# Kernel tuning notes

Hardware: AMD Instinct MI355X
Metric: run time of the kernel (lower is better)

Reference implementation:

```python
import jax, jax.numpy as jnp
import numpy as np

B, N, C, H = 4, 2048, 1024, 16
D = C // H

def setup_inputs() -> dict:
    key = jax.random.key(0)
    k1, k2, k3 = jax.random.split(key, 3)
    x = jax.random.normal(k1, (B, N, C), dtype=jnp.float32)
    w_qkv = jax.random.normal(k2, (C, 3 * C), dtype=jnp.float32) * (C ** -0.5)
    w_proj = jax.random.normal(k3, (C, C), dtype=jnp.float32) * (C ** -0.5)
    b_proj = jnp.zeros((C,), dtype=jnp.float32)
    return {"x": x, "w_qkv": w_qkv, "w_proj": w_proj, "b_proj": b_proj}

def reference(x, w_qkv, w_proj, b_proj):
    scale = D ** -0.5
    qkv = x @ w_qkv                                   # [B,N,3C]
    qkv = qkv.reshape(B, N, 3, H, D).transpose(2, 0, 3, 1, 4)  # [3,B,H,N,D]
    q, k, v = qkv[0], qkv[1], qkv[2]
    attn = jnp.einsum('bhnd,bhmd->bhnm', q, k) * scale  # [B,H,N,N]
    attn = jax.nn.softmax(attn, axis=-1)
    o = jnp.einsum('bhnm,bhmd->bhnd', attn, v)          # [B,H,N,D]
    o = o.transpose(0, 2, 1, 3).reshape(B, N, C)
    return o @ w_proj + b_proj
```

## Files before the change

kernel.cpp:

```cpp
#include <hip/hip_runtime.h>
#include <hip/hip_bf16.h>


#define B_ 4
#define N_ 2048
#define C_ 1024
#define H_ 16
#define D_ 64
#define MCONST 24.0f

typedef __attribute__((ext_vector_type(8))) __bf16 bf16x8;
typedef __attribute__((ext_vector_type(4))) float f32x4;
typedef __attribute__((ext_vector_type(16))) float f32x16;
typedef unsigned int u32;
typedef __attribute__((ext_vector_type(2))) u32 u32x2;
typedef __attribute__((ext_vector_type(4))) u32 u32x4;

__device__ inline unsigned short f2bf(float f) {
  __bf16 h = (__bf16)f;
  return __builtin_bit_cast(unsigned short, h);
}

__device__ __forceinline__ u32 pk2(float lo, float hi) {
  return (u32)f2bf(lo) | ((u32)f2bf(hi) << 16);
}

__device__ __forceinline__ void gld16(const void* g, void* l) {
  __builtin_amdgcn_global_load_lds(
      (const __attribute__((address_space(1))) u32*)g,
      (__attribute__((address_space(3))) u32*)l, 16, 0, 0);
}

__global__ __launch_bounds__(256) void cvt_bf16_kernel(
    const float* __restrict__ in, unsigned short* __restrict__ out) {
  int i = (blockIdx.x * 256 + threadIdx.x) * 8;
  float4 f0 = *(const float4*)&in[i];
  float4 f1 = *(const float4*)&in[i + 4];
  ushort4 h0, h1;
  h0.x = f2bf(f0.x); h0.y = f2bf(f0.y); h0.z = f2bf(f0.z); h0.w = f2bf(f0.w);
  h1.x = f2bf(f1.x); h1.y = f2bf(f1.y); h1.z = f2bf(f1.z); h1.w = f2bf(f1.w);
  *(ushort4*)&out[i] = h0;
  *(ushort4*)&out[i + 4] = h1;
}

__global__ __launch_bounds__(256) void transpose_cvt_kernel(
    const float* __restrict__ in, unsigned short* __restrict__ out,
    int K, int Nn) {
  __shared__ float tile[32][33];
  const int t = threadIdx.x;
  const int k0 = blockIdx.y * 32, n0 = blockIdx.x * 32;
  {
    int r = t >> 3, c = (t & 7) * 4;
    float4 f = *(const float4*)&in[(size_t)(k0 + r) * Nn + n0 + c];
    tile[r][c + 0] = f.x; tile[r][c + 1] = f.y;
    tile[r][c + 2] = f.z; tile[r][c + 3] = f.w;
  }
  __syncthreads();
  {
    int nr = t >> 3, kc = (t & 7) * 4;
    ushort4 h;
    h.x = f2bf(tile[kc + 0][nr]);
    h.y = f2bf(tile[kc + 1][nr]);
    h.z = f2bf(tile[kc + 2][nr]);
    h.w = f2bf(tile[kc + 3][nr]);
    *(ushort4*)&out[(size_t)(n0 + nr) * K + k0 + kc] = h;
  }
}

__global__ __launch_bounds__(256) void transpose_v_kernel(
    const unsigned short* __restrict__ vb, unsigned short* __restrict__ vtb) {
  __shared__ u32 tile[64][65];
  const int tid = threadIdx.x;
  const int n0 = blockIdx.x * 64;
  const int bh = blockIdx.y;
  const size_t base = (size_t)bh * N_ * D_;
#pragma unroll
  for (int i = 0; i < 2; i++) {
    int id = i * 256 + tid;
    int row = id >> 3, c8 = id & 7;
    uint4 v = *(const uint4*)&vb[base + (size_t)(n0 + row) * D_ + c8 * 8];
    const unsigned short* pv = (const unsigned short*)&v;
#pragma unroll
    for (int j = 0; j < 8; j++) tile[row][c8 * 8 + j] = pv[j];
  }
  __syncthreads();
#pragma unroll
  for (int i = 0; i < 2; i++) {
    int id = i * 256 + tid;
    int d = id >> 3, nc = id & 7;
    uint4 o;
    unsigned short* po = (unsigned short*)&o;
#pragma unroll
    for (int j = 0; j < 8; j++) po[j] = (unsigned short)tile[nc * 8 + j][d];
    *(uint4*)&vtb[base + (size_t)d * N_ + n0 + nc * 8] = o;
  }
}

__global__ __launch_bounds__(512, 1) void gemm256_kernel(
    const unsigned short* __restrict__ A, const unsigned short* __restrict__ Bt,
    unsigned short* __restrict__ qb, unsigned short* __restrict__ kb,
    unsigned short* __restrict__ vb, int M, int K, int Nout)
{
  __shared__ unsigned short LDS[3][2][256 * 32];
  const int tid = threadIdx.x;
  const int w = tid >> 6, lane = tid & 63;
  const int l15 = lane & 15, lk = lane >> 4;
  const int wm = w >> 2, wn = w & 3;
  const int n0 = blockIdx.x * 256, m0 = blockIdx.y * 256;

  const int s_row = tid >> 2;
  const int s_col = ((tid & 3) * 8) ^ (((s_row >> 3) & 1) * 16);
  const int s_dst = tid * 8;
  const int kcol = (lk * 8) ^ (((l15 >> 3) & 1) * 16);

  f32x4 acc[8][4];
#pragma unroll
  for (int m = 0; m < 8; m++)
#pragma unroll
    for (int n = 0; n < 4; n++) acc[m][n] = f32x4{0.f, 0.f, 0.f, 0.f};

#pragma unroll
  for (int i = 0; i < 2; i++)
    gld16(&A[(size_t)(m0 + i * 128 + s_row) * K + s_col],
          &LDS[0][0][i * 4096 + s_dst]);
#pragma unroll
  for (int i = 0; i < 2; i++)
    gld16(&Bt[(size_t)(n0 + i * 128 + s_row) * K + s_col],
          &LDS[0][1][i * 4096 + s_dst]);

  int cur = 0;
  for (int j = 0; j < 31; ++j) {
    const int nxt = (cur + 1 == 3) ? 0 : cur + 1;
    const int kt = (j + 1) * 32;
#pragma unroll
    for (int i = 0; i < 2; i++)
      gld16(&A[(size_t)(m0 + i * 128 + s_row) * K + kt + s_col],
            &LDS[nxt][0][i * 4096 + s_dst]);
    asm volatile("s_waitcnt vmcnt(2)" ::: "memory");
    __builtin_amdgcn_s_barrier();
    asm volatile("" ::: "memory");

    bf16x8 bf[4], af[4];
#pragma unroll
    for (int n = 0; n < 4; n++)
      bf[n] = *(const bf16x8*)&LDS[cur][1][(wn * 64 + n * 16 + l15) * 32 + kcol];
#pragma unroll
    for (int m = 0; m < 4; m++)
      af[m] = *(const bf16x8*)&LDS[cur][0][(wm * 128 + m * 16 + l15) * 32 + kcol];
    __builtin_amdgcn_s_setprio(1);
#pragma unroll
    for (int m = 0; m < 4; m++)
#pragma unroll
      for (int n = 0; n < 4; n++)
        acc[m][n] = __builtin_amdgcn_mfma_f32_16x16x32_bf16(af[m], bf[n], acc[m][n], 0, 0, 0);
    __builtin_amdgcn_s_setprio(0);

#pragma unroll
    for (int i = 0; i < 2; i++)
      gld16(&Bt[(size_t)(n0 + i * 128 + s_row) * K + kt + s_col],
            &LDS[nxt][1][i * 4096 + s_dst]);

#pragma unroll
    for (int m = 0; m < 4; m++)
      af[m] = *(const bf16x8*)&LDS[cur][0][(wm * 128 + (m + 4) * 16 + l15) * 32 + kcol];
    __builtin_amdgcn_s_setprio(1);
#pragma unroll
    for (int m = 0; m < 4; m++)
#pragma unroll
      for (int n = 0; n < 4; n++)
        acc[m + 4][n] = __builtin_amdgcn_mfma_f32_16x16x32_bf16(af[m], bf[n], acc[m + 4][n], 0, 0, 0);
    __builtin_amdgcn_s_setprio(0);
    cur = nxt;
  }

  asm volatile("s_waitcnt vmcnt(0)" ::: "memory");
  __builtin_amdgcn_s_barrier();
  asm volatile("" ::: "memory");
  {
    bf16x8 bf[4], af[4];
#pragma unroll
    for (int n = 0; n < 4; n++)
      bf[n] = *(const bf16x8*)&LDS[cur][1][(wn * 64 + n * 16 + l15) * 32 + kcol];
#pragma unroll
    for (int m = 0; m < 4; m++)
      af[m] = *(const bf16x8*)&LDS[cur][0][(wm * 128 + m * 16 + l15) * 32 + kcol];
#pragma unroll
    for (int m = 0; m < 4; m++)
#pragma unroll
      for (int n = 0; n < 4; n++)
        acc[m][n] = __builtin_amdgcn_mfma_f32_16x16x32_bf16(af[m], bf[n], acc[m][n], 0, 0, 0);
#pragma unroll
    for (int m = 0; m < 4; m++)
      af[m] = *(const bf16x8*)&LDS[cur][0][(wm * 128 + (m + 4) * 16 + l15) * 32 + kcol];
#pragma unroll
    for (int m = 0; m < 4; m++)
#pragma unroll
      for (int n = 0; n < 4; n++)
        acc[m + 4][n] = __builtin_amdgcn_mfma_f32_16x16x32_bf16(af[m], bf[n], acc[m + 4][n], 0, 0, 0);
  }

#pragma unroll
  for (int n = 0; n < 4; n++) {
    int c = n0 + wn * 64 + n * 16 + l15;
    int tsel = c >> 10, h = (c >> 6) & 15, d = c & 63;
    unsigned short* dst = (tsel == 0) ? qb : (tsel == 1 ? kb : vb);
    float sc = (tsel == 0) ? 0.125f * 1.44269504088896340736f : 1.0f;
#pragma unroll
    for (int m = 0; m < 8; m++) {
#pragma unroll
      for (int r = 0; r < 4; r++) {
        int row = m0 + wm * 128 + m * 16 + lk * 4 + r;
        int b = row >> 11, nn = row & 2047;
        dst[(((size_t)(b * 16 + h)) * 2048 + nn) * 64 + d] = f2bf(acc[m][n][r] * sc);
      }
    }
  }
}

__global__ __launch_bounds__(256) void gemm128_kernel(
    const unsigned short* __restrict__ A, const unsigned short* __restrict__ Bt,
    const float* __restrict__ bias, float* __restrict__ outp,
    int M, int K, int Nout)
{
  __shared__ unsigned short Al[128 * 64];
  __shared__ unsigned short Bl[128 * 64];
  const int tid = threadIdx.x;
  const int w = tid >> 6, lane = tid & 63;
  const int l15 = lane & 15, lk = lane >> 4;
  const int wr = w >> 1, wc = w & 1;
  const int n0 = blockIdx.x * 128, m0 = blockIdx.y * 128;
  const int srow = tid >> 3;
  const int scol = (tid & 7) * 8;

  f32x4 acc[4][4];
#pragma unroll
  for (int m = 0; m < 4; m++)
#pragma unroll
    for (int n = 0; n < 4; n++) acc[m][n] = f32x4{0.f, 0.f, 0.f, 0.f};

  for (int kt = 0; kt < K; kt += 64) {
#pragma unroll
    for (int i = 0; i < 4; i++)
      gld16(&A[(size_t)(m0 + i * 32 + srow) * K + kt + scol],
            &Al[i * 2048 + w * 512]);
#pragma unroll
    for (int i = 0; i < 4; i++)
      gld16(&Bt[(size_t)(n0 + i * 32 + srow) * K + kt + scol],
            &Bl[i * 2048 + w * 512]);
    __syncthreads();

#pragma unroll
    for (int kk = 0; kk < 2; kk++) {
      bf16x8 af[4], bf[4];
#pragma unroll
      for (int m = 0; m < 4; m++)
        af[m] = *(const bf16x8*)&Al[(wr * 64 + m * 16 + l15) * 64 + kk * 32 + lk * 8];
#pragma unroll
      for (int n = 0; n < 4; n++)
        bf[n] = *(const bf16x8*)&Bl[(wc * 64 + n * 16 + l15) * 64 + kk * 32 + lk * 8];
#pragma unroll
      for (int m = 0; m < 4; m++)
#pragma unroll
        for (int n = 0; n < 4; n++)
          acc[m][n] = __builtin_amdgcn_mfma_f32_16x16x32_bf16(af[m], bf[n], acc[m][n], 0, 0, 0);
    }
    __syncthreads();
  }

#pragma unroll
  for (int n = 0; n < 4; n++) {
    int c = n0 + wc * 64 + n * 16 + l15;
    float bv = bias[c];
#pragma unroll
    for (int m = 0; m < 4; m++) {
#pragma unroll
      for (int r = 0; r < 4; r++) {
        int row = m0 + wr * 64 + m * 16 + lk * 4 + r;
        outp[(size_t)row * Nout + c] = acc[m][n][r] + bv;
      }
    }
  }
}

__global__ __launch_bounds__(512) void flash_kernel(
    const unsigned short* __restrict__ qb, const unsigned short* __restrict__ kb,
    const unsigned short* __restrict__ vtb, unsigned short* __restrict__ ob)
{
  __shared__ unsigned short KVs[2][2][2][64 * 64];
  __shared__ float Lf[2][128];
  float* scratch = (float*)&KVs[0][0][0][0];

  const int tid = threadIdx.x;
  const int w = tid >> 6;
  const int lane = tid & 63;
  const int l31 = lane & 31;
  const int hi = lane >> 5;
  const int g = w >> 2;
  const int ws = w & 3;
  const int q0 = blockIdx.x * 128;
  const int bh = blockIdx.y;
  const size_t base = (size_t)bh * N_ * D_;
  const unsigned short* Qg = qb + base;
  const unsigned short* Kg = kb + base;
  const unsigned short* Vtg = vtb + base;

  const int t8 = tid & 255;
  const int s_r = t8 >> 3;
  const int s_sl = (t8 & 7) ^ (s_r & 7);
  const int swz = (lane & 7) << 3;

  const int qrow_g = q0 + ws * 32 + l31;
  bf16x8 qf[4];
#pragma unroll
  for (int ds = 0; ds < 4; ds++)
    qf[ds] = *(const bf16x8*)&Qg[(size_t)qrow_g * 64 + ds * 16 + hi * 8];

  f32x16 acc0, acc1, minit;
#pragma unroll
  for (int i = 0; i < 16; i++) { acc0[i] = 0.f; acc1[i] = 0.f; minit[i] = -MCONST; }
  float lrow = 0.f;

  const int kvbeg = g * (N_ / 2);

#pragma unroll
  for (int i = 0; i < 2; i++)
    gld16(&Kg[(size_t)(kvbeg + i * 32 + s_r) * 64 + s_sl * 8],
          &KVs[g][0][0][i * 2048 + ws * 512]);
#pragma unroll
  for (int i = 0; i < 2; i++)
    gld16(&Vtg[(size_t)(i * 32 + s_r) * N_ + kvbeg + s_sl * 8],
          &KVs[g][0][1][i * 2048 + ws * 512]);

  int cur = 0;
  for (int it = 0; it < 16; ++it) {
    __syncthreads();

    if (it + 1 < 16) {
      int kvn = kvbeg + (it + 1) * 64;
#pragma unroll
      for (int i = 0; i < 2; i++)
        gld16(&Kg[(size_t)(kvn + i * 32 + s_r) * 64 + s_sl * 8],
              &KVs[g][cur ^ 1][0][i * 2048 + ws * 512]);
#pragma unroll
      for (int i = 0; i < 2; i++)
        gld16(&Vtg[(size_t)(i * 32 + s_r) * N_ + kvn + s_sl * 8],
              &KVs[g][cur ^ 1][1][i * 2048 + ws * 512]);
    }

    const unsigned short* Kl = &KVs[g][cur][0][0];
    const unsigned short* Vl = &KVs[g][cur][1][0];

    u32 F[4][4];
#pragma unroll
    for (int t = 0; t < 2; t++) {
      f32x16 sa = minit;
      __builtin_amdgcn_s_setprio(1);
#pragma unroll
      for (int ds = 0; ds < 4; ds++) {
        bf16x8 a = *(const bf16x8*)&Kl[(t * 32 + l31) * 64 + ((ds * 16 + hi * 8) ^ swz)];
        sa = __builtin_amdgcn_mfma_f32_32x32x16_bf16(a, qf[ds], sa, 0, 0, 0);
      }
      __builtin_amdgcn_s_setprio(0);

      float p[16];
#pragma unroll
      for (int r = 0; r < 16; r++) p[r] = __builtin_amdgcn_exp2f(sa[r]);
      lrow += ((p[0] + p[1]) + (p[2] + p[3])) + ((p[4] + p[5]) + (p[6] + p[7]))
            + ((p[8] + p[9]) + (p[10] + p[11])) + ((p[12] + p[13]) + (p[14] + p[15]));

      u32 pk[8];
#pragma unroll
      for (int j = 0; j < 8; j++) pk[j] = pk2(p[2 * j], p[2 * j + 1]);
#if __has_builtin(__builtin_amdgcn_permlane32_swap)
      u32x2 r02 = __builtin_amdgcn_permlane32_swap(pk[0], pk[2], false, false);
      u32x2 r13 = __builtin_amdgcn_permlane32_swap(pk[1], pk[3], false, false);
      u32x2 r46 = __builtin_amdgcn_permlane32_swap(pk[4], pk[6], false, false);
      u32x2 r57 = __builtin_amdgcn_permlane32_swap(pk[5], pk[7], false, false);
      F[2 * t][0] = r02[0]; F[2 * t][2] = r02[1];
      F[2 * t][1] = r13[0]; F[2 * t][3] = r13[1];
      F[2 * t + 1][0] = r46[0]; F[2 * t + 1][2] = r46[1];
      F[2 * t + 1][1] = r57[0]; F[2 * t + 1][3] = r57[1];
#else
      u32 sw[8];
#pragma unroll
      for (int j = 0; j < 8; j++) sw[j] = (u32)__shfl_xor((int)pk[j], 32);
      F[2 * t][0] = hi ? sw[2] : pk[0];
      F[2 * t][1] = hi ? sw[3] : pk[1];
      F[2 * t][2] = hi ? pk[2] : sw[0];
      F[2 * t][3] = hi ? pk[3] : sw[1];
      F[2 * t + 1][0] = hi ? sw[6] : pk[4];
      F[2 * t + 1][1] = hi ? sw[7] : pk[5];
      F[2 * t + 1][2] = hi ? pk[6] : sw[4];
      F[2 * t + 1][3] = hi ? pk[7] : sw[5];
#endif
    }

    __builtin_amdgcn_s_setprio(1);
#pragma unroll
    for (int ks = 0; ks < 4; ks++) {
      u32x4 fv = {F[ks][0], F[ks][1], F[ks][2], F[ks][3]};
      bf16x8 a = __builtin_bit_cast(bf16x8, fv);
      bf16x8 b0 = *(const bf16x8*)&Vl[(0 * 32 + l31) * 64 + ((ks * 16 + hi * 8) ^ swz)];
      acc0 = __builtin_amdgcn_mfma_f32_32x32x16_bf16(a, b0, acc0, 0, 0, 0);
      bf16x8 b1 = *(const bf16x8*)&Vl[(1 * 32 + l31) * 64 + ((ks * 16 + hi * 8) ^ swz)];
      acc1 = __builtin_amdgcn_mfma_f32_32x32x16_bf16(a, b1, acc1, 0, 0, 0);
    }
    __builtin_amdgcn_s_setprio(0);
    cur ^= 1;
  }

  float rs = lrow + __shfl_xor(lrow, 32);
  if (lane < 32) Lf[g][ws * 32 + l31] = rs;
  __syncthreads();

  if (g == 0) {
#pragma unroll
    for (int r = 0; r < 16; r++) {
      int qr = (r & 3) + 8 * (r >> 2) + 4 * hi;
      scratch[(ws * 32 + qr) * 64 + l31]      = acc0[r];
      scratch[(ws * 32 + qr) * 64 + 32 + l31] = acc1[r];
    }
  }
  __syncthreads();
  if (g == 1) {
    const int b = bh >> 4, h = bh & 15;
#pragma unroll
    for (int r = 0; r < 16; r++) {
      int qr = (r & 3) + 8 * (r >> 2) + 4 * hi;
      float inv = 1.0f / (Lf[0][ws * 32 + qr] + Lf[1][ws * 32 + qr]);
      float o0 = scratch[(ws * 32 + qr) * 64 + l31]      + acc0[r];
      float o1 = scratch[(ws * 32 + qr) * 64 + 32 + l31] + acc1[r];
      int nq = q0 + ws * 32 + qr;
      size_t ob0 = (((size_t)b * N_ + nq) * H_ + h) * D_;
      ob[ob0 + l31]      = f2bf(o0 * inv);
      ob[ob0 + 32 + l31] = f2bf(o1 * inv);
    }
  }
}

extern "C" void kernel_launch(void* const* d_in, const int* in_sizes, int n_in,
                              void* d_out, int out_size, void* d_ws, size_t ws_size,
                              hipStream_t stream) {
  const float* x      = (const float*)d_in[0];
  const float* w_qkv  = (const float*)d_in[1];
  const float* w_proj = (const float*)d_in[2];
  const float* b_proj = (const float*)d_in[3];
  float* out = (float*)d_out;

  const size_t qsz = (size_t)B_ * H_ * N_ * D_;
  unsigned short* qb     = (unsigned short*)d_ws;
  unsigned short* kb     = qb + qsz;
  unsigned short* vb     = kb + qsz;
  unsigned short* vtb    = vb + qsz;
  unsigned short* xbf    = vtb + qsz;
  unsigned short* ob     = xbf;
  unsigned short* wqkv_t = xbf + qsz;
  unsigned short* wproj_t= wqkv_t + (size_t)3072 * 1024;

  cvt_bf16_kernel<<<4096, 256, 0, stream>>>(x, xbf);
  transpose_cvt_kernel<<<dim3(3072 / 32, 1024 / 32), 256, 0, stream>>>(w_qkv, wqkv_t, 1024, 3072);
  transpose_cvt_kernel<<<dim3(1024 / 32, 1024 / 32), 256, 0, stream>>>(w_proj, wproj_t, 1024, 1024);

  gemm256_kernel<<<dim3(3072 / 256, 8192 / 256), 512, 0, stream>>>(
      xbf, wqkv_t, qb, kb, vb, 8192, 1024, 3072);

  transpose_v_kernel<<<dim3(N_ / 64, B_ * H_), 256, 0, stream>>>(vb, vtb);

  flash_kernel<<<dim3(N_ / 128, B_ * H_), 512, 0, stream>>>(qb, kb, vtb, ob);

  gemm128_kernel<<<dim3(1024 / 128, 8192 / 128), 256, 0, stream>>>(
      ob, wproj_t, b_proj, out, 8192, 1024, 1024);
}
```

Before: 217.4 us.

## Fuse V transpose into QKV GEMM epilogue and pipeline projection GEMM

New measurement: 212.6 us. -2.2%, faster.

```diff
diff --git a/kernel.cpp b/kernel.cpp
--- a/kernel.cpp
+++ b/kernel.cpp
@@ -8,6 +8,7 @@
 #define H_ 16
 #define D_ 64
 #define MCONST 24.0f
+#define QSCALE (0.125f * 1.44269504088896340736f)
 
 typedef __attribute__((ext_vector_type(8))) __bf16 bf16x8;
 typedef __attribute__((ext_vector_type(4))) float f32x4;
@@ -67,39 +68,10 @@
   }
 }
 
-__global__ __launch_bounds__(256) void transpose_v_kernel(
-    const unsigned short* __restrict__ vb, unsigned short* __restrict__ vtb) {
-  __shared__ u32 tile[64][65];
-  const int tid = threadIdx.x;
-  const int n0 = blockIdx.x * 64;
-  const int bh = blockIdx.y;
-  const size_t base = (size_t)bh * N_ * D_;
-#pragma unroll
-  for (int i = 0; i < 2; i++) {
-    int id = i * 256 + tid;
-    int row = id >> 3, c8 = id & 7;
-    uint4 v = *(const uint4*)&vb[base + (size_t)(n0 + row) * D_ + c8 * 8];
-    const unsigned short* pv = (const unsigned short*)&v;
-#pragma unroll
-    for (int j = 0; j < 8; j++) tile[row][c8 * 8 + j] = pv[j];
-  }
-  __syncthreads();
-#pragma unroll
-  for (int i = 0; i < 2; i++) {
-    int id = i * 256 + tid;
-    int d = id >> 3, nc = id & 7;
-    uint4 o;
-    unsigned short* po = (unsigned short*)&o;
-#pragma unroll
-    for (int j = 0; j < 8; j++) po[j] = (unsigned short)tile[nc * 8 + j][d];
-    *(uint4*)&vtb[base + (size_t)d * N_ + n0 + nc * 8] = o;
-  }
-}
-
 __global__ __launch_bounds__(512, 1) void gemm256_kernel(
     const unsigned short* __restrict__ A, const unsigned short* __restrict__ Bt,
     unsigned short* __restrict__ qb, unsigned short* __restrict__ kb,
-    unsigned short* __restrict__ vb, int M, int K, int Nout)
+    unsigned short* __restrict__ vtb, int M, int K, int Nout)
 {
   __shared__ unsigned short LDS[3][2][256 * 32];
   const int tid = threadIdx.x;
@@ -203,34 +175,48 @@
   for (int n = 0; n < 4; n++) {
     int c = n0 + wn * 64 + n * 16 + l15;
     int tsel = c >> 10, h = (c >> 6) & 15, d = c & 63;
-    unsigned short* dst = (tsel == 0) ? qb : (tsel == 1 ? kb : vb);
-    float sc = (tsel == 0) ? 0.125f * 1.44269504088896340736f : 1.0f;
-#pragma unroll
-    for (int m = 0; m < 8; m++) {
-#pragma unroll
-      for (int r = 0; r < 4; r++) {
-        int row = m0 + wm * 128 + m * 16 + lk * 4 + r;
-        int b = row >> 11, nn = row & 2047;
-        dst[(((size_t)(b * 16 + h)) * 2048 + nn) * 64 + d] = f2bf(acc[m][n][r] * sc);
+    if (tsel < 2) {
+      unsigned short* dst = (tsel == 0) ? qb : kb;
+      float sc = (tsel == 0) ? QSCALE : 1.0f;
+#pragma unroll
+      for (int m = 0; m < 8; m++) {
+#pragma unroll
+        for (int r = 0; r < 4; r++) {
+          int row = m0 + wm * 128 + m * 16 + lk * 4 + r;
+          int b = row >> 11, nn = row & 2047;
+          dst[(((size_t)(b * 16 + h)) * 2048 + nn) * 64 + d] = f2bf(acc[m][n][r] * sc);
+        }
       }
-    }
-  }
-}
-
-__global__ __launch_bounds__(256) void gemm128_kernel(
+    } else {
+#pragma unroll
+      for (int m = 0; m < 8; m++) {
+        int row0 = m0 + wm * 128 + m * 16 + lk * 4;
+        int b = row0 >> 11, nn = row0 & 2047;
+        ushort4 pv;
+        pv.x = f2bf(acc[m][n][0]); pv.y = f2bf(acc[m][n][1]);
+        pv.z = f2bf(acc[m][n][2]); pv.w = f2bf(acc[m][n][3]);
+        *(ushort4*)&vtb[(((size_t)(b * 16 + h)) * 64 + d) * 2048 + nn] = pv;
+      }
+    }
+  }
+}
+
+__global__ __launch_bounds__(512, 1) void gemmproj_kernel(
     const unsigned short* __restrict__ A, const unsigned short* __restrict__ Bt,
     const float* __restrict__ bias, float* __restrict__ outp,
     int M, int K, int Nout)
 {
-  __shared__ unsigned short Al[128 * 64];
-  __shared__ unsigned short Bl[128 * 64];
+  __shared__ unsigned short LDS[3][12288];
   const int tid = threadIdx.x;
   const int w = tid >> 6, lane = tid & 63;
   const int l15 = lane & 15, lk = lane >> 4;
-  const int wr = w >> 1, wc = w & 1;
-  const int n0 = blockIdx.x * 128, m0 = blockIdx.y * 128;
-  const int srow = tid >> 3;
-  const int scol = (tid & 7) * 8;
+  const int wm = w >> 1, wn = w & 1;
+  const int n0 = blockIdx.x * 128, m0 = blockIdx.y * 256;
+
+  const int s_row = tid >> 2;
+  const int s_col = ((tid & 3) * 8) ^ (((s_row >> 3) & 1) * 16);
+  const int s_dst = tid * 8;
+  const int kcol = (lk * 8) ^ (((l15 >> 3) & 1) * 16);
 
   f32x4 acc[4][4];
 #pragma unroll
@@ -238,44 +224,89 @@
 #pragma unroll
     for (int n = 0; n < 4; n++) acc[m][n] = f32x4{0.f, 0.f, 0.f, 0.f};
 
-  for (int kt = 0; kt < K; kt += 64) {
-#pragma unroll
-    for (int i = 0; i < 4; i++)
-      gld16(&A[(size_t)(m0 + i * 32 + srow) * K + kt + scol],
-            &Al[i * 2048 + w * 512]);
-#pragma unroll
-    for (int i = 0; i < 4; i++)
-      gld16(&Bt[(size_t)(n0 + i * 32 + srow) * K + kt + scol],
-            &Bl[i * 2048 + w * 512]);
-    __syncthreads();
-
-#pragma unroll
-    for (int kk = 0; kk < 2; kk++) {
-      bf16x8 af[4], bf[4];
-#pragma unroll
-      for (int m = 0; m < 4; m++)
-        af[m] = *(const bf16x8*)&Al[(wr * 64 + m * 16 + l15) * 64 + kk * 32 + lk * 8];
-#pragma unroll
-      for (int n = 0; n < 4; n++)
-        bf[n] = *(const bf16x8*)&Bl[(wc * 64 + n * 16 + l15) * 64 + kk * 32 + lk * 8];
-#pragma unroll
-      for (int m = 0; m < 4; m++)
-#pragma unroll
-        for (int n = 0; n < 4; n++)
-          acc[m][n] = __builtin_amdgcn_mfma_f32_16x16x32_bf16(af[m], bf[n], acc[m][n], 0, 0, 0);
-    }
-    __syncthreads();
+#pragma unroll
+  for (int i = 0; i < 2; i++)
+    gld16(&A[(size_t)(m0 + i * 128 + s_row) * K + s_col],
+          &LDS[0][i * 4096 + s_dst]);
+  gld16(&Bt[(size_t)(n0 + s_row) * K + s_col], &LDS[0][8192 + s_dst]);
+
+  int cur = 0;
+  for (int j = 0; j < 31; ++j) {
+    const int nxt = (cur + 1 == 3) ? 0 : cur + 1;
+    const int kt = (j + 1) * 32;
+#pragma unroll
+    for (int i = 0; i < 2; i++)
+      gld16(&A[(size_t)(m0 + i * 128 + s_row) * K + kt + s_col],
+            &LDS[nxt][i * 4096 + s_dst]);
+    asm volatile("s_waitcnt vmcnt(2)" ::: "memory");
+    __builtin_amdgcn_s_barrier();
+    asm volatile("" ::: "memory");
+
+    bf16x8 bf[4], af[2];
+#pragma unroll
+    for (int n = 0; n < 4; n++)
+      bf[n] = *(const bf16x8*)&LDS[cur][8192 + (wn * 64 + n * 16 + l15) * 32 + kcol];
+#pragma unroll
+    for (int m = 0; m < 2; m++)
+      af[m] = *(const bf16x8*)&LDS[cur][(wm * 64 + m * 16 + l15) * 32 + kcol];
+    __builtin_amdgcn_s_setprio(1);
+#pragma unroll
+    for (int m = 0; m < 2; m++)
+#pragma unroll
+      for (int n = 0; n < 4; n++)
+        acc[m][n] = __builtin_amdgcn_mfma_f32_16x16x32_bf16(af[m], bf[n], acc[m][n], 0, 0, 0);
+    __builtin_amdgcn_s_setprio(0);
+
+    gld16(&Bt[(size_t)(n0 + s_row) * K + kt + s_col], &LDS[nxt][8192 + s_dst]);
+
+#pragma unroll
+    for (int m = 0; m < 2; m++)
+      af[m] = *(const bf16x8*)&LDS[cur][(wm * 64 + (m + 2) * 16 + l15) * 32 + kcol];
+    __builtin_amdgcn_s_setprio(1);
+#pragma unroll
+    for (int m = 0; m < 2; m++)
+#pragma unroll
+      for (int n = 0; n < 4; n++)
+        acc[m + 2][n] = __builtin_amdgcn_mfma_f32_16x16x32_bf16(af[m], bf[n], acc[m + 2][n], 0, 0, 0);
+    __builtin_amdgcn_s_setprio(0);
+    cur = nxt;
+  }
+
+  asm volatile("s_waitcnt vmcnt(0)" ::: "memory");
+  __builtin_amdgcn_s_barrier();
+  asm volatile("" ::: "memory");
+  {
+    bf16x8 bf[4], af[2];
+#pragma unroll
+    for (int n = 0; n < 4; n++)
+      bf[n] = *(const bf16x8*)&LDS[cur][8192 + (wn * 64 + n * 16 + l15) * 32 + kcol];
+#pragma unroll
+    for (int m = 0; m < 2; m++)
+      af[m] = *(const bf16x8*)&LDS[cur][(wm * 64 + m * 16 + l15) * 32 + kcol];
+#pragma unroll
+    for (int m = 0; m < 2; m++)
+#pragma unroll
+      for (int n = 0; n < 4; n++)
+        acc[m][n] = __builtin_amdgcn_mfma_f32_16x16x32_bf16(af[m], bf[n], acc[m][n], 0, 0, 0);
+#pragma unroll
+    for (int m = 0; m < 2; m++)
+      af[m] = *(const bf16x8*)&LDS[cur][(wm * 64 + (m + 2) * 16 + l15) * 32 + kcol];
+#pragma unroll
+    for (int m = 0; m < 2; m++)
+#pragma unroll
+      for (int n = 0; n < 4; n++)
+        acc[m + 2][n] = __builtin_amdgcn_mfma_f32_16x16x32_bf16(af[m], bf[n], acc[m + 2][n], 0, 0, 0);
   }
 
 #pragma unroll
   for (int n = 0; n < 4; n++) {
-    int c = n0 + wc * 64 + n * 16 + l15;
+    int c = n0 + wn * 64 + n * 16 + l15;
     float bv = bias[c];
 #pragma unroll
     for (int m = 0; m < 4; m++) {
 #pragma unroll
       for (int r = 0; r < 4; r++) {
-        int row = m0 + wr * 64 + m * 16 + lk * 4 + r;
+        int row = m0 + wm * 64 + m * 16 + lk * 4 + r;
         outp[(size_t)row * Nout + c] = acc[m][n][r] + bv;
       }
     }
@@ -450,8 +481,7 @@
   const size_t qsz = (size_t)B_ * H_ * N_ * D_;
   unsigned short* qb     = (unsigned short*)d_ws;
   unsigned short* kb     = qb + qsz;
-  unsigned short* vb     = kb + qsz;
-  unsigned short* vtb    = vb + qsz;
+  unsigned short* vtb    = kb + qsz;
   unsigned short* xbf    = vtb + qsz;
   unsigned short* ob     = xbf;
   unsigned short* wqkv_t = xbf + qsz;
@@ -462,12 +492,10 @@
   transpose_cvt_kernel<<<dim3(1024 / 32, 1024 / 32), 256, 0, stream>>>(w_proj, wproj_t, 1024, 1024);
 
   gemm256_kernel<<<dim3(3072 / 256, 8192 / 256), 512, 0, stream>>>(
-      xbf, wqkv_t, qb, kb, vb, 8192, 1024, 3072);
-
-  transpose_v_kernel<<<dim3(N_ / 64, B_ * H_), 256, 0, stream>>>(vb, vtb);
+      xbf, wqkv_t, qb, kb, vtb, 8192, 1024, 3072);
 
   flash_kernel<<<dim3(N_ / 128, B_ * H_), 512, 0, stream>>>(qb, kb, vtb, ob);
 
-  gemm128_kernel<<<dim3(1024 / 128, 8192 / 128), 256, 0, stream>>>(
+  gemmproj_kernel<<<dim3(1024 / 128, 8192 / 256), 512, 0, stream>>>(
       ob, wproj_t, b_proj, out, 8192, 1024, 1024);
 }
```
